# Kernel optimization log

Hardware: AMD Instinct MI355X
Metric: run time of the kernel (lower is better)

Reference implementation:

```python
import jax, jax.numpy as jnp
import numpy as np

D = 1024  # dim_context


def setup_inputs() -> dict:
    key = jax.random.key(0)
    k1, k2, k3, k4, k5 = jax.random.split(key, 5)
    B, T = 32, 2048
    hidden = jax.random.normal(k1, (B, D), dtype=jnp.float32)
    encoder_outputs = jax.random.normal(k2, (B, T, D), dtype=jnp.float32)
    # nn.Linear(2D, D): weight [D, 2D], bias [D]
    lim = 1.0 / np.sqrt(2 * D)
    W = jax.random.uniform(k3, (D, 2 * D), minval=-lim, maxval=lim, dtype=jnp.float32)
    b = jax.random.uniform(k4, (D,), minval=-lim, maxval=lim, dtype=jnp.float32)
    stdv = 1.0 / np.sqrt(D)
    v = jax.random.uniform(k5, (D,), minval=-stdv, maxval=stdv, dtype=jnp.float32)
    return {"hidden": hidden, "encoder_outputs": encoder_outputs, "W": W, "b": b, "v": v}


def reference(hidden, encoder_outputs, W, b, v):
    # hidden: [B, D]; encoder_outputs: [B, T, D]
    B, T, Dm = encoder_outputs.shape
    h = jnp.broadcast_to(hidden[:, None, :], (B, T, Dm))      # repeat over T
    attn_inputs = jnp.concatenate([h, encoder_outputs], axis=2)  # [B, T, 2D]
    energy = jax.nn.relu(jnp.einsum('btk,dk->btd', attn_inputs, W) + b)  # [B, T, D]
    scores = jnp.einsum('btd,d->bt', energy, v)                # [B, T]
    # softmax over dim=1 (time axis), then unsqueeze(1)
    return jax.nn.softmax(scores, axis=1)[:, None, :]          # [B, 1, T]
```

## Files before the change

kernel.cpp:

```cpp
#include <hip/hip_runtime.h>
#include <cstdint>


#define GLOBAL_AS __attribute__((address_space(1)))
#define LDS_AS    __attribute__((address_space(3)))

typedef __bf16 bf16x8 __attribute__((ext_vector_type(8)));
typedef float  f32x4  __attribute__((ext_vector_type(4)));

__device__ __forceinline__ unsigned int f2bf(float x) {
    unsigned int u = __builtin_bit_cast(unsigned int, x);
    u += 0x7fffu + ((u >> 16) & 1u);
    return u >> 16;
}

__global__ __launch_bounds__(256) void k_convert_enc(const float4* __restrict__ in,
                                                     uint4* __restrict__ out) {
    size_t idx = (size_t)blockIdx.x * 256 + threadIdx.x;
    float4 f0 = in[idx * 2];
    float4 f1 = in[idx * 2 + 1];
    uint4 o;
    o.x = f2bf(f0.x) | (f2bf(f0.y) << 16);
    o.y = f2bf(f0.z) | (f2bf(f0.w) << 16);
    o.z = f2bf(f1.x) | (f2bf(f1.y) << 16);
    o.w = f2bf(f1.z) | (f2bf(f1.w) << 16);
    out[idx] = o;
}

__global__ __launch_bounds__(256) void k_convert_we(const float* __restrict__ W,
                                                    uint2* __restrict__ out) {
    int idx = blockIdx.x * 256 + threadIdx.x;
    int i = idx * 4;
    int n = i >> 10, k = i & 1023;
    const float4 f = *(const float4*)(W + (size_t)n * 2048 + 1024 + k);
    uint2 o;
    o.x = f2bf(f.x) | (f2bf(f.y) << 16);
    o.y = f2bf(f.z) | (f2bf(f.w) << 16);
    out[idx] = o;
}

__global__ __launch_bounds__(256) void k_hidden_proj(const float* __restrict__ hidden,
                                                     const float* __restrict__ W,
                                                     const float* __restrict__ bias,
                                                     float* __restrict__ u) {
    __shared__ float wrow[1024];
    __shared__ float red[256];
    const int tid = threadIdx.x, d = blockIdx.x;
    ((float4*)wrow)[tid] = ((const float4*)(W + (size_t)d * 2048))[tid];
    __syncthreads();
    const int b = tid & 31, kc = tid >> 5;
    const float* h = hidden + b * 1024 + kc * 128;
    const float* w = wrow + kc * 128;
    float acc = 0.f;
    #pragma unroll 8
    for (int i = 0; i < 128; i += 4) {
        float4 hv = *(const float4*)(h + i);
        acc += w[i] * hv.x + w[i + 1] * hv.y + w[i + 2] * hv.z + w[i + 3] * hv.w;
    }
    red[tid] = acc;
    __syncthreads();
    if (tid < 32) {
        float s = 0.f;
        #pragma unroll
        for (int j = 0; j < 8; j++) s += red[j * 32 + tid];
        u[tid * 1024 + d] = s + bias[d];
    }
}

__global__ __launch_bounds__(256, 4) void k_gemm_score(
        const unsigned short* __restrict__ Ab,
        const unsigned short* __restrict__ Bw,
        const float* __restrict__ u,
        const float* __restrict__ v,
        float* __restrict__ scores2) {
    constexpr int K = 1024, BK = 64;
    __shared__ __align__(16) unsigned short As[128 * BK];
    __shared__ __align__(16) unsigned short Bs[128 * BK];
    __shared__ float red[2][128];

    const int tid  = threadIdx.x;
    const int wave = tid >> 6;
    const int lane = tid & 63;
    const int mb   = blockIdx.x;
    const int z    = blockIdx.y;
    const int wm = wave & 1, wn = wave >> 1;
    const int q = lane >> 4, cl = lane & 15;

    int aoff[4], boff[4];
    #pragma unroll
    for (int i = 0; i < 4; i++) {
        int ra = wm * 64 + i * 16 + cl;
        aoff[i] = ra * 64 + ((q ^ (ra & 7)) << 3);
        int rb = wn * 64 + i * 16 + cl;
        boff[i] = rb * 64 + ((q ^ (rb & 7)) << 3);
    }

    int soff[4];
    #pragma unroll
    for (int c = 0; c < 4; c++) {
        int row = (wave * 4 + c) * 8 + (lane >> 3);
        int g   = (lane & 7) ^ (row & 7);
        soff[c] = row * K + g * 8;
    }
    const unsigned short* Abase = Ab + (size_t)(mb * 128) * K;

    float sacc[4][4];
    #pragma unroll
    for (int i = 0; i < 4; i++)
        #pragma unroll
        for (int r = 0; r < 4; r++) sacc[i][r] = 0.f;

    const int bidx = mb >> 4;
    f32x4 acc[4][4];

    for (int p = 0; p < 4; p++) {
        const int nb = z * 4 + p;
        const unsigned short* Bbase = Bw + (size_t)(nb * 128) * K;
        #pragma unroll
        for (int i = 0; i < 4; i++)
            #pragma unroll
            for (int j = 0; j < 4; j++) acc[i][j] = (f32x4){0.f, 0.f, 0.f, 0.f};

        for (int k0 = 0; k0 < K; k0 += BK) {
            #pragma unroll
            for (int c = 0; c < 4; c++) {
                const int chunk = wave * 4 + c;
                __builtin_amdgcn_global_load_lds(
                    (GLOBAL_AS void*)(size_t)(Abase + soff[c] + k0),
                    (LDS_AS void*)(As + chunk * 512), 16, 0, 0);
                __builtin_amdgcn_global_load_lds(
                    (GLOBAL_AS void*)(size_t)(Bbase + soff[c] + k0),
                    (LDS_AS void*)(Bs + chunk * 512), 16, 0, 0);
            }
            __syncthreads();
            #pragma unroll
            for (int h = 0; h < 2; h++) {
                const int hx = h * 32;
                bf16x8 afr[4], bfr[4];
                #pragma unroll
                for (int i = 0; i < 4; i++) afr[i] = *(const bf16x8*)(As + (aoff[i] ^ hx));
                #pragma unroll
                for (int j = 0; j < 4; j++) bfr[j] = *(const bf16x8*)(Bs + (boff[j] ^ hx));
                #pragma unroll
                for (int i = 0; i < 4; i++)
                    #pragma unroll
                    for (int j = 0; j < 4; j++)
                        acc[i][j] = __builtin_amdgcn_mfma_f32_16x16x32_bf16(afr[i], bfr[j], acc[i][j], 0, 0, 0);
            }
            __syncthreads();
        }

        float vv[4], uu[4];
        #pragma unroll
        for (int j = 0; j < 4; j++) {
            int n = nb * 128 + wn * 64 + j * 16 + cl;
            vv[j] = v[n];
            uu[j] = u[bidx * 1024 + n];
        }
        #pragma unroll
        for (int i = 0; i < 4; i++)
            #pragma unroll
            for (int r = 0; r < 4; r++) {
                float s = sacc[i][r];
                #pragma unroll
                for (int j = 0; j < 4; j++)
                    s += fmaxf(acc[i][j][r] + uu[j], 0.f) * vv[j];
                sacc[i][r] = s;
            }
    }

    #pragma unroll
    for (int i = 0; i < 4; i++)
        #pragma unroll
        for (int r = 0; r < 4; r++) {
            float s = sacc[i][r];
            s += __shfl_xor(s, 1);
            s += __shfl_xor(s, 2);
            s += __shfl_xor(s, 4);
            s += __shfl_xor(s, 8);
            if (cl == 0) red[wn][wm * 64 + i * 16 + q * 4 + r] = s;
        }
    __syncthreads();
    if (tid < 128) scores2[(size_t)z * 65536 + mb * 128 + tid] = red[0][tid] + red[1][tid];
}

__global__ __launch_bounds__(256) void k_softmax(const float* __restrict__ scores2,
                                                 float* __restrict__ out) {
    __shared__ float red[4];
    int b = blockIdx.x;
    int t0 = threadIdx.x;
    int wave = threadIdx.x >> 6, lane = threadIdx.x & 63;
    const float* s0 = scores2 + b * 2048;
    const float* s1 = scores2 + 65536 + b * 2048;
    float vals[8];
    float lmax = -1e30f;
    #pragma unroll
    for (int i = 0; i < 8; i++) {
        int t = t0 + i * 256;
        vals[i] = s0[t] + s1[t];
        lmax = fmaxf(lmax, vals[i]);
    }
    for (int o = 32; o > 0; o >>= 1) lmax = fmaxf(lmax, __shfl_xor(lmax, o));
    if (lane == 0) red[wave] = lmax;
    __syncthreads();
    float gmax = fmaxf(fmaxf(red[0], red[1]), fmaxf(red[2], red[3]));
    float lsum = 0.f;
    #pragma unroll
    for (int i = 0; i < 8; i++) {
        vals[i] = expf(vals[i] - gmax);
        lsum += vals[i];
    }
    for (int o = 32; o > 0; o >>= 1) lsum += __shfl_xor(lsum, o);
    __syncthreads();
    if (lane == 0) red[wave] = lsum;
    __syncthreads();
    float inv = 1.0f / (red[0] + red[1] + red[2] + red[3]);
    #pragma unroll
    for (int i = 0; i < 8; i++) out[b * 2048 + t0 + i * 256] = vals[i] * inv;
}

extern "C" void kernel_launch(void* const* d_in, const int* in_sizes, int n_in,
                              void* d_out, int out_size, void* d_ws, size_t ws_size,
                              hipStream_t stream) {
    const float* hidden = (const float*)d_in[0];
    const float* enc    = (const float*)d_in[1];
    const float* W      = (const float*)d_in[2];
    const float* bias   = (const float*)d_in[3];
    const float* v      = (const float*)d_in[4];
    float* out = (float*)d_out;

    char* ws = (char*)d_ws;
    unsigned short* encb = (unsigned short*)ws;
    unsigned short* Web  = (unsigned short*)(ws + 134217728);
    float* u       = (float*)(ws + 134217728 + 2097152);
    float* scores2 = (float*)(ws + 134217728 + 2097152 + 131072);

    k_convert_enc<<<32768, 256, 0, stream>>>((const float4*)enc, (uint4*)encb);
    k_convert_we<<<1024, 256, 0, stream>>>(W, (uint2*)Web);
    k_hidden_proj<<<1024, 256, 0, stream>>>(hidden, W, bias, u);
    dim3 g(512, 2);
    k_gemm_score<<<g, 256, 0, stream>>>(encb, Web, u, v, scores2);
    k_softmax<<<32, 256, 0, stream>>>(scores2, out);
}
```

Measured before the change: 559.3 us.

## Rewrite score GEMM with 256x256 tiles, double-buffered LDS and phased MFMA schedule

Reworks the fused GEMM+score kernel to use 512-thread blocks computing 256-row tiles across all 1024 output columns (256-column passes). The two-way N split and the partial-score sum in softmax go away. Global-to-LDS loads are double-buffered and interleaved with MFMA phases, using explicit waitcnt, barriers and setprio to overlap memory with compute. This raises operand reuse per LDS load and hides load latency. In exchange it uses more LDS and registers per block, and launches only 256 blocks, which lowers occupancy and wave-level parallelism.

```diff
diff --git a/kernel.cpp b/kernel.cpp
--- a/kernel.cpp
+++ b/kernel.cpp
@@ -67,98 +67,148 @@
     }
 }
 
-__global__ __launch_bounds__(256, 4) void k_gemm_score(
+
+#define STAGE_A(S, h, kk) do {                                                          \
+    __builtin_amdgcn_global_load_lds(                                                   \
+        (GLOBAL_AS void*)(size_t)(Ab + arow0 + (kk) + (h) * 32),                        \
+        (LDS_AS void*)(&As[S][h][c0 * 512]), 16, 0, 0);                                 \
+    __builtin_amdgcn_global_load_lds(                                                   \
+        (GLOBAL_AS void*)(size_t)(Ab + arow1 + (kk) + (h) * 32),                        \
+        (LDS_AS void*)(&As[S][h][c0 * 512 + 512]), 16, 0, 0);                           \
+} while (0)
+
+#define STAGE_B(S, h, kk, nbn) do {                                                     \
+    __builtin_amdgcn_global_load_lds(                                                   \
+        (GLOBAL_AS void*)(size_t)(Bw + (size_t)(nbn) * 262144 + brow0 + (kk) + (h) * 32), \
+        (LDS_AS void*)(&Bs[S][h][c0 * 512]), 16, 0, 0);                                 \
+    __builtin_amdgcn_global_load_lds(                                                   \
+        (GLOBAL_AS void*)(size_t)(Bw + (size_t)(nbn) * 262144 + brow1 + (kk) + (h) * 32), \
+        (LDS_AS void*)(&Bs[S][h][c0 * 512 + 512]), 16, 0, 0);                           \
+} while (0)
+
+#define PHASE_MFMA(jp)                                                                  \
+    __builtin_amdgcn_s_barrier();                                                       \
+    asm volatile("s_waitcnt lgkmcnt(0)" ::: "memory");                                  \
+    __builtin_amdgcn_sched_barrier(0);                                                  \
+    __builtin_amdgcn_s_setprio(1);                                                      \
+    _Pragma("unroll")                                                                   \
+    for (int i = 0; i < 8; i++) {                                                       \
+        acc[i][2 * (jp)]     = __builtin_amdgcn_mfma_f32_16x16x32_bf16(                 \
+            afr[i], bfr[0], acc[i][2 * (jp)], 0, 0, 0);                                 \
+        acc[i][2 * (jp) + 1] = __builtin_amdgcn_mfma_f32_16x16x32_bf16(                 \
+            afr[i], bfr[1], acc[i][2 * (jp) + 1], 0, 0, 0);                             \
+    }                                                                                   \
+    __builtin_amdgcn_s_setprio(0);                                                      \
+    __builtin_amdgcn_s_barrier();
+
+#define TILE(C, S, kst, nbn) do {                                                       \
+    {                                                               \
+        const unsigned short* Ap = As[C][0];                                            \
+        const unsigned short* Bp = Bs[C][0];                                            \
+        _Pragma("unroll")                                                               \
+        for (int i = 0; i < 8; i++) afr[i] = *(const bf16x8*)(Ap + aBase + i * 512);    \
+        bfr[0] = *(const bf16x8*)(Bp + bBase);                                          \
+        bfr[1] = *(const bf16x8*)(Bp + bBase + 512);                                    \
+        STAGE_A(S, 0, kst);                                                             \
+        PHASE_MFMA(0)                                                                   \
+    }                                                                                   \
+    {                                                               \
+        const unsigned short* Bp = Bs[C][0];                                            \
+        bfr[0] = *(const bf16x8*)(Bp + bBase + 1024);                                   \
+        bfr[1] = *(const bf16x8*)(Bp + bBase + 1536);                                   \
+        STAGE_B(S, 0, kst, nbn);                                                        \
+        asm volatile("s_waitcnt vmcnt(4)" ::: "memory");                                \
+        PHASE_MFMA(1)                                                                   \
+    }                                                                                   \
+    {                                                               \
+        const unsigned short* Ap = As[C][1];                                            \
+        const unsigned short* Bp = Bs[C][1];                                            \
+        _Pragma("unroll")                                                               \
+        for (int i = 0; i < 8; i++) afr[i] = *(const bf16x8*)(Ap + aBase + i * 512);    \
+        bfr[0] = *(const bf16x8*)(Bp + bBase);                                          \
+        bfr[1] = *(const bf16x8*)(Bp + bBase + 512);                                    \
+        STAGE_A(S, 1, kst);                                                             \
+        PHASE_MFMA(0)                                                                   \
+    }                                                                                   \
+    {                                                               \
+        const unsigned short* Bp = Bs[C][1];                                            \
+        bfr[0] = *(const bf16x8*)(Bp + bBase + 1024);                                   \
+        bfr[1] = *(const bf16x8*)(Bp + bBase + 1536);                                   \
+        STAGE_B(S, 1, kst, nbn);                                                        \
+        asm volatile("s_waitcnt vmcnt(4)" ::: "memory");                                \
+        PHASE_MFMA(1)                                                                   \
+    }                                                                                   \
+} while (0)
+
+__global__ __launch_bounds__(512, 2) void k_gemm_score(
         const unsigned short* __restrict__ Ab,
         const unsigned short* __restrict__ Bw,
         const float* __restrict__ u,
         const float* __restrict__ v,
-        float* __restrict__ scores2) {
-    constexpr int K = 1024, BK = 64;
-    __shared__ __align__(16) unsigned short As[128 * BK];
-    __shared__ __align__(16) unsigned short Bs[128 * BK];
-    __shared__ float red[2][128];
+        float* __restrict__ scores) {
+    __shared__ __align__(16) unsigned short As[2][2][8192];
+    __shared__ __align__(16) unsigned short Bs[2][2][8192];
+    __shared__ float red[4][256];
 
     const int tid  = threadIdx.x;
     const int wave = tid >> 6;
     const int lane = tid & 63;
     const int mb   = blockIdx.x;
-    const int z    = blockIdx.y;
     const int wm = wave & 1, wn = wave >> 1;
     const int q = lane >> 4, cl = lane & 15;
-
-    int aoff[4], boff[4];
-    #pragma unroll
-    for (int i = 0; i < 4; i++) {
-        int ra = wm * 64 + i * 16 + cl;
-        aoff[i] = ra * 64 + ((q ^ (ra & 7)) << 3);
-        int rb = wn * 64 + i * 16 + cl;
-        boff[i] = rb * 64 + ((q ^ (rb & 7)) << 3);
-    }
-
-    int soff[4];
-    #pragma unroll
-    for (int c = 0; c < 4; c++) {
-        int row = (wave * 4 + c) * 8 + (lane >> 3);
-        int g   = (lane & 7) ^ (row & 7);
-        soff[c] = row * K + g * 8;
-    }
-    const unsigned short* Abase = Ab + (size_t)(mb * 128) * K;
-
-    float sacc[4][4];
-    #pragma unroll
-    for (int i = 0; i < 4; i++)
+    const int bidx = mb >> 3;
+
+    const int perm  = (q ^ ((cl >> 1) & 3)) << 3;
+    const int aBase = (wm * 128 + cl) * 32 + perm;
+    const int bBase = (wn * 64 + cl) * 32 + perm;
+
+    const int c0 = wave * 2;
+    const int g8 = (((lane & 3) ^ ((lane >> 3) & 3)) << 3);
+    const int rowA0 = c0 * 16 + (lane >> 2);
+    const size_t arow0 = (size_t)(mb * 256 + rowA0) * 1024 + g8;
+    const size_t arow1 = arow0 + 16 * 1024;
+    const size_t brow0 = (size_t)rowA0 * 1024 + g8;
+    const size_t brow1 = brow0 + 16 * 1024;
+
+    f32x4 acc[8][4];
+    float sacc[8][4];
+    bf16x8 afr[8], bfr[2];
+    #pragma unroll
+    for (int i = 0; i < 8; i++)
         #pragma unroll
         for (int r = 0; r < 4; r++) sacc[i][r] = 0.f;
 
-    const int bidx = mb >> 4;
-    f32x4 acc[4][4];
+    STAGE_A(0, 0, 0);
+    STAGE_B(0, 0, 0, 0);
+    STAGE_A(0, 1, 0);
+    STAGE_B(0, 1, 0, 0);
+    asm volatile("s_waitcnt vmcnt(4)" ::: "memory");
+    __builtin_amdgcn_s_barrier();
 
     for (int p = 0; p < 4; p++) {
-        const int nb = z * 4 + p;
-        const unsigned short* Bbase = Bw + (size_t)(nb * 128) * K;
-        #pragma unroll
-        for (int i = 0; i < 4; i++)
+        #pragma unroll
+        for (int i = 0; i < 8; i++)
             #pragma unroll
             for (int j = 0; j < 4; j++) acc[i][j] = (f32x4){0.f, 0.f, 0.f, 0.f};
 
-        for (int k0 = 0; k0 < K; k0 += BK) {
-            #pragma unroll
-            for (int c = 0; c < 4; c++) {
-                const int chunk = wave * 4 + c;
-                __builtin_amdgcn_global_load_lds(
-                    (GLOBAL_AS void*)(size_t)(Abase + soff[c] + k0),
-                    (LDS_AS void*)(As + chunk * 512), 16, 0, 0);
-                __builtin_amdgcn_global_load_lds(
-                    (GLOBAL_AS void*)(size_t)(Bbase + soff[c] + k0),
-                    (LDS_AS void*)(Bs + chunk * 512), 16, 0, 0);
-            }
-            __syncthreads();
-            #pragma unroll
-            for (int h = 0; h < 2; h++) {
-                const int hx = h * 32;
-                bf16x8 afr[4], bfr[4];
-                #pragma unroll
-                for (int i = 0; i < 4; i++) afr[i] = *(const bf16x8*)(As + (aoff[i] ^ hx));
-                #pragma unroll
-                for (int j = 0; j < 4; j++) bfr[j] = *(const bf16x8*)(Bs + (boff[j] ^ hx));
-                #pragma unroll
-                for (int i = 0; i < 4; i++)
-                    #pragma unroll
-                    for (int j = 0; j < 4; j++)
-                        acc[i][j] = __builtin_amdgcn_mfma_f32_16x16x32_bf16(afr[i], bfr[j], acc[i][j], 0, 0, 0);
-            }
-            __syncthreads();
+        for (int it = 0; it < 8; it++) {
+            const int k1 = (2 * it + 1) * 64;
+            TILE(0, 1, k1, p);
+            const int last = (it == 7);
+            const int k2  = last ? 0 : (2 * it + 2) * 64;
+            const int nb2 = last ? ((p < 3) ? p + 1 : 3) : p;
+            TILE(1, 0, k2, nb2);
         }
 
         float vv[4], uu[4];
         #pragma unroll
         for (int j = 0; j < 4; j++) {
-            int n = nb * 128 + wn * 64 + j * 16 + cl;
+            int n = p * 256 + wn * 64 + j * 16 + cl;
             vv[j] = v[n];
             uu[j] = u[bidx * 1024 + n];
         }
         #pragma unroll
-        for (int i = 0; i < 4; i++)
+        for (int i = 0; i < 8; i++)
             #pragma unroll
             for (int r = 0; r < 4; r++) {
                 float s = sacc[i][r];
@@ -170,7 +220,7 @@
     }
 
     #pragma unroll
-    for (int i = 0; i < 4; i++)
+    for (int i = 0; i < 8; i++)
         #pragma unroll
         for (int r = 0; r < 4; r++) {
             float s = sacc[i][r];
@@ -178,26 +228,28 @@
             s += __shfl_xor(s, 2);
             s += __shfl_xor(s, 4);
             s += __shfl_xor(s, 8);
-            if (cl == 0) red[wn][wm * 64 + i * 16 + q * 4 + r] = s;
+            if (cl == 0) red[wn][wm * 128 + i * 16 + q * 4 + r] = s;
         }
     __syncthreads();
-    if (tid < 128) scores2[(size_t)z * 65536 + mb * 128 + tid] = red[0][tid] + red[1][tid];
-}
-
-__global__ __launch_bounds__(256) void k_softmax(const float* __restrict__ scores2,
+    if (tid < 256) {
+        scores[(size_t)mb * 256 + tid] =
+            red[0][tid] + red[1][tid] + red[2][tid] + red[3][tid];
+    }
+}
+
+__global__ __launch_bounds__(256) void k_softmax(const float* __restrict__ scores,
                                                  float* __restrict__ out) {
     __shared__ float red[4];
     int b = blockIdx.x;
     int t0 = threadIdx.x;
     int wave = threadIdx.x >> 6, lane = threadIdx.x & 63;
-    const float* s0 = scores2 + b * 2048;
-    const float* s1 = scores2 + 65536 + b * 2048;
+    const float* s0 = scores + b * 2048;
     float vals[8];
     float lmax = -1e30f;
     #pragma unroll
     for (int i = 0; i < 8; i++) {
         int t = t0 + i * 256;
-        vals[i] = s0[t] + s1[t];
+        vals[i] = s0[t];
         lmax = fmaxf(lmax, vals[i]);
     }
     for (int o = 32; o > 0; o >>= 1) lmax = fmaxf(lmax, __shfl_xor(lmax, o));
@@ -232,13 +284,12 @@
     char* ws = (char*)d_ws;
     unsigned short* encb = (unsigned short*)ws;
     unsigned short* Web  = (unsigned short*)(ws + 134217728);
-    float* u       = (float*)(ws + 134217728 + 2097152);
-    float* scores2 = (float*)(ws + 134217728 + 2097152 + 131072);
+    float* u      = (float*)(ws + 134217728 + 2097152);
+    float* scores = (float*)(ws + 134217728 + 2097152 + 131072);
 
     k_convert_enc<<<32768, 256, 0, stream>>>((const float4*)enc, (uint4*)encb);
     k_convert_we<<<1024, 256, 0, stream>>>(W, (uint2*)Web);
     k_hidden_proj<<<1024, 256, 0, stream>>>(hidden, W, bias, u);
-    dim3 g(512, 2);
-    k_gemm_score<<<g, 256, 0, stream>>>(encb, Web, u, v, scores2);
-    k_softmax<<<32, 256, 0, stream>>>(scores2, out);
-}
+    k_gemm_score<<<256, 512, 0, stream>>>(encb, Web, u, v, scores);
+    k_softmax<<<32, 256, 0, stream>>>(scores, out);
+}
```

Result: slower. 575.7 us (+2.9%).

## Fuse fp32-to-bf16 conversion of encoder outputs into GEMM A-tile loads

Applied to the files above, without the earlier changes.

Drops the separate encoder conversion pass, which wrote a 128MB bf16 copy, and has the GEMM read fp32 encoder rows directly, converting them to bf16 in registers before storing to LDS. The next A tile is prefetched into registers while the MFMAs run. The W-half conversion moves into the hidden-projection kernel. The grid changes from 512x2 blocks, each looping over 4 N-tiles, to 4096 blocks that each own one (M,N) tile with a swizzled mapping, so there are 8 partial score buffers, which the softmax now sums. Each block re-reads fp32 A for its N-tile, so A is read 8 times from memory or cache, and register pressure rises (launch bounds lowered to 3).

```diff
diff --git a/kernel.cpp b/kernel.cpp
--- a/kernel.cpp
+++ b/kernel.cpp
@@ -14,38 +14,21 @@
     return u >> 16;
 }
 
-__global__ __launch_bounds__(256) void k_convert_enc(const float4* __restrict__ in,
-                                                     uint4* __restrict__ out) {
-    size_t idx = (size_t)blockIdx.x * 256 + threadIdx.x;
-    float4 f0 = in[idx * 2];
-    float4 f1 = in[idx * 2 + 1];
-    uint4 o;
-    o.x = f2bf(f0.x) | (f2bf(f0.y) << 16);
-    o.y = f2bf(f0.z) | (f2bf(f0.w) << 16);
-    o.z = f2bf(f1.x) | (f2bf(f1.y) << 16);
-    o.w = f2bf(f1.z) | (f2bf(f1.w) << 16);
-    out[idx] = o;
-}
-
-__global__ __launch_bounds__(256) void k_convert_we(const float* __restrict__ W,
-                                                    uint2* __restrict__ out) {
-    int idx = blockIdx.x * 256 + threadIdx.x;
-    int i = idx * 4;
-    int n = i >> 10, k = i & 1023;
-    const float4 f = *(const float4*)(W + (size_t)n * 2048 + 1024 + k);
-    uint2 o;
-    o.x = f2bf(f.x) | (f2bf(f.y) << 16);
-    o.y = f2bf(f.z) | (f2bf(f.w) << 16);
-    out[idx] = o;
-}
-
 __global__ __launch_bounds__(256) void k_hidden_proj(const float* __restrict__ hidden,
                                                      const float* __restrict__ W,
                                                      const float* __restrict__ bias,
-                                                     float* __restrict__ u) {
+                                                     float* __restrict__ u,
+                                                     uint2* __restrict__ Web) {
     __shared__ float wrow[1024];
     __shared__ float red[256];
     const int tid = threadIdx.x, d = blockIdx.x;
+    {
+        const float4 wf = *(const float4*)(W + (size_t)d * 2048 + 1024 + tid * 4);
+        uint2 o;
+        o.x = f2bf(wf.x) | (f2bf(wf.y) << 16);
+        o.y = f2bf(wf.z) | (f2bf(wf.w) << 16);
+        Web[d * 256 + tid] = o;
+    }
     ((float4*)wrow)[tid] = ((const float4*)(W + (size_t)d * 2048))[tid];
     __syncthreads();
     const int b = tid & 31, kc = tid >> 5;
@@ -67,12 +50,12 @@
     }
 }
 
-__global__ __launch_bounds__(256, 4) void k_gemm_score(
-        const unsigned short* __restrict__ Ab,
+__global__ __launch_bounds__(256, 3) void k_gemm_score(
+        const float* __restrict__ Af,
         const unsigned short* __restrict__ Bw,
         const float* __restrict__ u,
         const float* __restrict__ v,
-        float* __restrict__ scores2) {
+        float* __restrict__ scores8) {
     constexpr int K = 1024, BK = 64;
     __shared__ __align__(16) unsigned short As[128 * BK];
     __shared__ __align__(16) unsigned short Bs[128 * BK];
@@ -81,8 +64,10 @@
     const int tid  = threadIdx.x;
     const int wave = tid >> 6;
     const int lane = tid & 63;
-    const int mb   = blockIdx.x;
-    const int z    = blockIdx.y;
+    const int bid  = blockIdx.x;
+    const int lg   = (bid & 7) * 512 + (bid >> 3);
+    const int mb   = lg >> 3;
+    const int nb   = lg & 7;
     const int wm = wave & 1, wn = wave >> 1;
     const int q = lane >> 4, cl = lane & 15;
 
@@ -95,85 +80,91 @@
         boff[i] = rb * 64 + ((q ^ (rb & 7)) << 3);
     }
 
-    int soff[4];
+    int soffB[4];
     #pragma unroll
     for (int c = 0; c < 4; c++) {
         int row = (wave * 4 + c) * 8 + (lane >> 3);
         int g   = (lane & 7) ^ (row & 7);
-        soff[c] = row * K + g * 8;
-    }
-    const unsigned short* Abase = Ab + (size_t)(mb * 128) * K;
-
-    float sacc[4][4];
+        soffB[c] = row * K + g * 8;
+    }
+    const unsigned short* Bbase = Bw + (size_t)(nb * 128) * K;
+
+    const int ar  = tid >> 1;
+    const int ac0 = (tid & 1) * 32;
+    const float* Arow = Af + (size_t)(mb * 128 + ar) * K + ac0;
+    int awoff[4];
+    #pragma unroll
+    for (int g = 0; g < 4; g++) {
+        int G = (tid & 1) * 4 + g;
+        awoff[g] = ar * 64 + ((G ^ (ar & 7)) << 3);
+    }
+
+    const int bidx = mb >> 4;
+
+    float4 aL[8];
+    #pragma unroll
+    for (int x = 0; x < 8; x++) aL[x] = *(const float4*)(Arow + x * 4);
+
+    f32x4 acc[4][4];
     #pragma unroll
     for (int i = 0; i < 4; i++)
         #pragma unroll
-        for (int r = 0; r < 4; r++) sacc[i][r] = 0.f;
-
-    const int bidx = mb >> 4;
-    f32x4 acc[4][4];
-
-    for (int p = 0; p < 4; p++) {
-        const int nb = z * 4 + p;
-        const unsigned short* Bbase = Bw + (size_t)(nb * 128) * K;
-        #pragma unroll
-        for (int i = 0; i < 4; i++)
-            #pragma unroll
-            for (int j = 0; j < 4; j++) acc[i][j] = (f32x4){0.f, 0.f, 0.f, 0.f};
-
-        for (int k0 = 0; k0 < K; k0 += BK) {
-            #pragma unroll
-            for (int c = 0; c < 4; c++) {
-                const int chunk = wave * 4 + c;
-                __builtin_amdgcn_global_load_lds(
-                    (GLOBAL_AS void*)(size_t)(Abase + soff[c] + k0),
-                    (LDS_AS void*)(As + chunk * 512), 16, 0, 0);
-                __builtin_amdgcn_global_load_lds(
-                    (GLOBAL_AS void*)(size_t)(Bbase + soff[c] + k0),
-                    (LDS_AS void*)(Bs + chunk * 512), 16, 0, 0);
-            }
-            __syncthreads();
-            #pragma unroll
-            for (int h = 0; h < 2; h++) {
-                const int hx = h * 32;
-                bf16x8 afr[4], bfr[4];
-                #pragma unroll
-                for (int i = 0; i < 4; i++) afr[i] = *(const bf16x8*)(As + (aoff[i] ^ hx));
-                #pragma unroll
-                for (int j = 0; j < 4; j++) bfr[j] = *(const bf16x8*)(Bs + (boff[j] ^ hx));
-                #pragma unroll
-                for (int i = 0; i < 4; i++)
-                    #pragma unroll
-                    for (int j = 0; j < 4; j++)
-                        acc[i][j] = __builtin_amdgcn_mfma_f32_16x16x32_bf16(afr[i], bfr[j], acc[i][j], 0, 0, 0);
-            }
-            __syncthreads();
-        }
-
-        float vv[4], uu[4];
-        #pragma unroll
-        for (int j = 0; j < 4; j++) {
-            int n = nb * 128 + wn * 64 + j * 16 + cl;
-            vv[j] = v[n];
-            uu[j] = u[bidx * 1024 + n];
-        }
-        #pragma unroll
-        for (int i = 0; i < 4; i++)
-            #pragma unroll
-            for (int r = 0; r < 4; r++) {
-                float s = sacc[i][r];
+        for (int j = 0; j < 4; j++) acc[i][j] = (f32x4){0.f, 0.f, 0.f, 0.f};
+
+    for (int k0 = 0; k0 < K; k0 += BK) {
+        #pragma unroll
+        for (int g = 0; g < 4; g++) {
+            float4 lo = aL[2 * g], hi = aL[2 * g + 1];
+            bf16x8 w;
+            w[0] = (__bf16)lo.x; w[1] = (__bf16)lo.y; w[2] = (__bf16)lo.z; w[3] = (__bf16)lo.w;
+            w[4] = (__bf16)hi.x; w[5] = (__bf16)hi.y; w[6] = (__bf16)hi.z; w[7] = (__bf16)hi.w;
+            *(bf16x8*)(As + awoff[g]) = w;
+        }
+        #pragma unroll
+        for (int c = 0; c < 4; c++)
+            __builtin_amdgcn_global_load_lds(
+                (GLOBAL_AS void*)(size_t)(Bbase + soffB[c] + k0),
+                (LDS_AS void*)(Bs + (wave * 4 + c) * 512), 16, 0, 0);
+        __syncthreads();
+
+        if (k0 + BK < K) {
+            #pragma unroll
+            for (int x = 0; x < 8; x++)
+                aL[x] = *(const float4*)(Arow + (k0 + BK) + x * 4);
+        }
+
+        #pragma unroll
+        for (int h = 0; h < 2; h++) {
+            const int hx = h * 32;
+            bf16x8 afr[4], bfr[4];
+            #pragma unroll
+            for (int i = 0; i < 4; i++) afr[i] = *(const bf16x8*)(As + (aoff[i] ^ hx));
+            #pragma unroll
+            for (int j = 0; j < 4; j++) bfr[j] = *(const bf16x8*)(Bs + (boff[j] ^ hx));
+            #pragma unroll
+            for (int i = 0; i < 4; i++)
                 #pragma unroll
                 for (int j = 0; j < 4; j++)
-                    s += fmaxf(acc[i][j][r] + uu[j], 0.f) * vv[j];
-                sacc[i][r] = s;
-            }
-    }
-
+                    acc[i][j] = __builtin_amdgcn_mfma_f32_16x16x32_bf16(afr[i], bfr[j], acc[i][j], 0, 0, 0);
+        }
+        __syncthreads();
+    }
+
+    float vv[4], uu[4];
+    #pragma unroll
+    for (int j = 0; j < 4; j++) {
+        int n = nb * 128 + wn * 64 + j * 16 + cl;
+        vv[j] = v[n];
+        uu[j] = u[bidx * 1024 + n];
+    }
     #pragma unroll
     for (int i = 0; i < 4; i++)
         #pragma unroll
         for (int r = 0; r < 4; r++) {
-            float s = sacc[i][r];
+            float s = 0.f;
+            #pragma unroll
+            for (int j = 0; j < 4; j++)
+                s += fmaxf(acc[i][j][r] + uu[j], 0.f) * vv[j];
             s += __shfl_xor(s, 1);
             s += __shfl_xor(s, 2);
             s += __shfl_xor(s, 4);
@@ -181,23 +172,25 @@
             if (cl == 0) red[wn][wm * 64 + i * 16 + q * 4 + r] = s;
         }
     __syncthreads();
-    if (tid < 128) scores2[(size_t)z * 65536 + mb * 128 + tid] = red[0][tid] + red[1][tid];
-}
-
-__global__ __launch_bounds__(256) void k_softmax(const float* __restrict__ scores2,
+    if (tid < 128) scores8[(size_t)nb * 65536 + mb * 128 + tid] = red[0][tid] + red[1][tid];
+}
+
+__global__ __launch_bounds__(256) void k_softmax(const float* __restrict__ scores8,
                                                  float* __restrict__ out) {
     __shared__ float red[4];
     int b = blockIdx.x;
     int t0 = threadIdx.x;
     int wave = threadIdx.x >> 6, lane = threadIdx.x & 63;
-    const float* s0 = scores2 + b * 2048;
-    const float* s1 = scores2 + 65536 + b * 2048;
+    const float* s0 = scores8 + b * 2048;
     float vals[8];
     float lmax = -1e30f;
     #pragma unroll
     for (int i = 0; i < 8; i++) {
         int t = t0 + i * 256;
-        vals[i] = s0[t] + s1[t];
+        float s = 0.f;
+        #pragma unroll
+        for (int qd = 0; qd < 8; qd++) s += s0[(size_t)qd * 65536 + t];
+        vals[i] = s;
         lmax = fmaxf(lmax, vals[i]);
     }
     for (int o = 32; o > 0; o >>= 1) lmax = fmaxf(lmax, __shfl_xor(lmax, o));
@@ -230,15 +223,11 @@
     float* out = (float*)d_out;
 
     char* ws = (char*)d_ws;
-    unsigned short* encb = (unsigned short*)ws;
-    unsigned short* Web  = (unsigned short*)(ws + 134217728);
-    float* u       = (float*)(ws + 134217728 + 2097152);
-    float* scores2 = (float*)(ws + 134217728 + 2097152 + 131072);
-
-    k_convert_enc<<<32768, 256, 0, stream>>>((const float4*)enc, (uint4*)encb);
-    k_convert_we<<<1024, 256, 0, stream>>>(W, (uint2*)Web);
-    k_hidden_proj<<<1024, 256, 0, stream>>>(hidden, W, bias, u);
-    dim3 g(512, 2);
-    k_gemm_score<<<g, 256, 0, stream>>>(encb, Web, u, v, scores2);
-    k_softmax<<<32, 256, 0, stream>>>(scores2, out);
-}
+    unsigned short* Web = (unsigned short*)ws;
+    float* u       = (float*)(ws + 2097152);
+    float* scores8 = (float*)(ws + 2097152 + 131072);
+
+    k_hidden_proj<<<1024, 256, 0, stream>>>(hidden, W, bias, u, (uint2*)Web);
+    k_gemm_score<<<4096, 256, 0, stream>>>(enc, Web, u, v, scores8);
+    k_softmax<<<32, 256, 0, stream>>>(scores8, out);
+}
```

After: 605.7 us. 1.08x slower.
